# Kernel tuning notes

Measured on AMD Instinct MI355X. Metric: run time of the kernel, lower is better.

## Reference

```python
import jax, jax.numpy as jnp
import numpy as np

E = 200000
T = 1000000
D = 128          # embed_dim
NB = 20          # n_basis (use_sh=False -> SimpleMLPAngleExpansion)


def setup_inputs() -> dict:
    key = jax.random.key(0)
    ks = jax.random.split(key, 16)
    s = lambda fan_in: 1.0 / np.sqrt(fan_in)
    return {
        "edge_attr": jax.random.normal(ks[0], (E, D), dtype=jnp.float32),
        "three_body_indices": jax.random.randint(ks[1], (T, 3), 0, 50000),
        "three_body_edge_indices": jax.random.randint(ks[2], (T, 2), 0, E),
        "edge_vectors": jax.random.normal(ks[3], (E, 3), dtype=jnp.float32),
        # SimpleMLPAngleExpansion: (len_ij, len_ik, cos) -> n_basis via 2-layer MLP
        "A1": jax.random.uniform(ks[4], (3, NB), jnp.float32, -s(3), s(3)),
        "ab1": jnp.zeros((NB,), jnp.float32),
        "A2": jax.random.uniform(ks[5], (NB, NB), jnp.float32, -s(NB), s(NB)),
        "ab2": jnp.zeros((NB,), jnp.float32),
        # phi_3b: Linear(2D+NB, D) -> SiLU -> Linear(D, D)
        "W1": jax.random.uniform(ks[6], (2 * D + NB, D), jnp.float32, -s(2 * D + NB), s(2 * D + NB)),
        "b1": jnp.zeros((D,), jnp.float32),
        "W2": jax.random.uniform(ks[7], (D, D), jnp.float32, -s(D), s(D)),
        "b2": jnp.zeros((D,), jnp.float32),
        # update_edge: Linear(D, D)
        "Wu": jax.random.uniform(ks[8], (D, D), jnp.float32, -s(D), s(D)),
        "bu": jnp.zeros((D,), jnp.float32),
    }


def reference(edge_attr, three_body_indices, three_body_edge_indices, edge_vectors,
              A1, ab1, A2, ab2, W1, b1, W2, b2, Wu, bu):
    e_ij = three_body_edge_indices[:, 0]
    e_ik = three_body_edge_indices[:, 1]
    vec_ij = -edge_vectors[e_ij]          # (T, 3)
    vec_ik = -edge_vectors[e_ik]          # (T, 3)
    len_ij = jnp.clip(jnp.linalg.norm(vec_ij, axis=1, keepdims=True), 1e-6)
    len_ik = jnp.clip(jnp.linalg.norm(vec_ik, axis=1, keepdims=True), 1e-6)
    cos = jnp.clip(jnp.sum(vec_ij * vec_ik, axis=1, keepdims=True) / (len_ij * len_ik), -1.0, 1.0)
    # angle expansion (SimpleMLPAngleExpansion): small MLP on geometric scalars
    f = jnp.concatenate([len_ij, len_ik, cos], axis=-1)       # (T, 3)
    angle_feats = jax.nn.silu(f @ A1 + ab1) @ A2 + ab2         # (T, NB)
    h_3b = jnp.concatenate([edge_attr[e_ij], edge_attr[e_ik], angle_feats], axis=-1)  # (T, 2D+NB)
    m_ijk = jax.nn.silu(h_3b @ W1 + b1) @ W2 + b2              # (T, D)
    delta = jax.ops.segment_sum(m_ijk, e_ij, num_segments=edge_attr.shape[0])  # (E, D)
    return delta @ Wu + bu
```

## Files before the change

### kernel.cpp

```cpp
#include <hip/hip_runtime.h>
#include <stdint.h>

#define D_ 128
#define NB_ 20
#define SCAN_B 1024
#define SEG_BLOCKS 2048
#define NWAVES (SEG_BLOCKS * 256 / 64)

typedef __bf16 bf16x8 __attribute__((ext_vector_type(8)));
typedef float f32x4 __attribute__((ext_vector_type(4)));
typedef float f32x2 __attribute__((ext_vector_type(2)));

__device__ __forceinline__ float silu_f(float x) {
  return x * __builtin_amdgcn_rcpf(1.0f + __expf(-x));
}
__device__ __forceinline__ f32x2 silu2(f32x2 x) {
  return (f32x2){silu_f(x.x), silu_f(x.y)};
}
__device__ __forceinline__ f32x2 fsplat(float x) { return (f32x2){x, x}; }

__device__ __forceinline__ float bf2f(unsigned short u) {
  return __uint_as_float(((unsigned int)u) << 16);
}
__device__ __forceinline__ unsigned short f2bf(float f) {
  unsigned int x = __float_as_uint(f);
  return (unsigned short)((x + 0x7fffu + ((x >> 16) & 1u)) >> 16);
}

__global__ __launch_bounds__(256) void prep_kernel(
    const float* __restrict__ A2, const float* __restrict__ ab2,
    const float* __restrict__ W1, const float* __restrict__ b1,
    const float* __restrict__ W2, const float* __restrict__ Wu,
    const float* __restrict__ b2,
    float* __restrict__ Mfold, float* __restrict__ b1p,
    unsigned short* __restrict__ W2uT, float* __restrict__ c2,
    unsigned short* __restrict__ W1T) {
  int tid = blockIdx.x * blockDim.x + threadIdx.x;
  if (tid < 21 * D_) {
    int r = tid >> 7, c = tid & (D_ - 1);
    if (r < NB_) {
      float acc = 0.f;
      for (int j = 0; j < NB_; ++j) acc += A2[r * NB_ + j] * W1[(2 * D_ + j) * D_ + c];
      Mfold[r * D_ + c] = acc;
    } else {
      float acc = b1[c];
      for (int j = 0; j < NB_; ++j) acc += ab2[j] * W1[(2 * D_ + j) * D_ + c];
      b1p[c] = acc;
    }
  } else if (tid < 2688 + 16384) {
    int i = tid - 2688;
    int n = i >> 7, k = i & 127;
    float acc = 0.f;
    for (int m = 0; m < D_; ++m) acc += W2[k * D_ + m] * Wu[m * D_ + n];
    W2uT[i] = f2bf(acc);
  } else if (tid < 19072 + 128) {
    int n = tid - 19072;
    float acc = 0.f;
    for (int m = 0; m < D_; ++m) acc += b2[m] * Wu[m * D_ + n];
    c2[n] = acc;
  } else if (tid < 19200 + 32768) {
    int i = tid - 19200;
    int r = i >> 7, k = i & 127;
    int half = r >> 7, n = r & 127;
    W1T[i] = f2bf(W1[(size_t)(half * 128 + k) * D_ + n]);
  }
}

__global__ __launch_bounds__(256) void pq_mfma(const float* __restrict__ edge_attr,
                                               const unsigned short* __restrict__ W1T,
                                               unsigned short* __restrict__ P,
                                               unsigned short* __restrict__ Q, int E) {
  const int lane = threadIdx.x & 63;
  const int wave = threadIdx.x >> 6;
  const int e0 = (blockIdx.x * 4 + wave) * 16;
  if (e0 >= E) return;
  const int row = lane & 15;
  const int quad = lane >> 4;
  int e = e0 + row; if (e >= E) e = E - 1;

  union { bf16x8 v; unsigned short u[8]; } afr[4];
  const float* arow = edge_attr + (size_t)e * D_ + quad * 8;
#pragma unroll
  for (int kt = 0; kt < 4; ++kt) {
    float4 f0 = *(const float4*)(arow + kt * 32);
    float4 f1 = *(const float4*)(arow + kt * 32 + 4);
    afr[kt].u[0] = f2bf(f0.x); afr[kt].u[1] = f2bf(f0.y);
    afr[kt].u[2] = f2bf(f0.z); afr[kt].u[3] = f2bf(f0.w);
    afr[kt].u[4] = f2bf(f1.x); afr[kt].u[5] = f2bf(f1.y);
    afr[kt].u[6] = f2bf(f1.z); afr[kt].u[7] = f2bf(f1.w);
  }
#pragma unroll
  for (int half = 0; half < 2; ++half) {
    unsigned short* Obase = half ? Q : P;
#pragma unroll
    for (int nt = 0; nt < 8; ++nt) {
      const unsigned short* wrow =
          W1T + ((size_t)(half * 128 + nt * 16 + row)) * 128 + quad * 8;
      f32x4 acc = {0.f, 0.f, 0.f, 0.f};
#pragma unroll
      for (int kt = 0; kt < 4; ++kt) {
        bf16x8 bfr = *(const bf16x8*)(wrow + kt * 32);
        acc = __builtin_amdgcn_mfma_f32_16x16x32_bf16(afr[kt].v, bfr, acc, 0, 0, 0);
      }
      int n = nt * 16 + row;
#pragma unroll
      for (int i = 0; i < 4; ++i) {
        int er = e0 + quad * 4 + i;
        if (er < E) Obase[(size_t)er * D_ + n] = f2bf(acc[i]);
      }
    }
  }
}

__global__ void hist_kernel(const int* __restrict__ tbe, int* __restrict__ cnt, int T_) {
  int t = blockIdx.x * blockDim.x + threadIdx.x;
  if (t < T_) atomicAdd(&cnt[((const int2*)tbe)[t].x], 1);
}

__global__ __launch_bounds__(SCAN_B) void scan1_kernel(const int* __restrict__ cnt,
                                                       int* __restrict__ pre,
                                                       int* __restrict__ bsum, int E) {
  __shared__ int lds[SCAN_B];
  int tid = threadIdx.x, i = blockIdx.x * SCAN_B + tid;
  int v = (i < E) ? cnt[i] : 0;
  lds[tid] = v;
  __syncthreads();
  for (int d = 1; d < SCAN_B; d <<= 1) {
    int add = (tid >= d) ? lds[tid - d] : 0;
    __syncthreads();
    lds[tid] += add;
    __syncthreads();
  }
  if (i < E) pre[i] = lds[tid] - v;
  if (tid == SCAN_B - 1) bsum[blockIdx.x] = lds[tid];
}

__global__ void scan2_kernel(int* __restrict__ bsum, int nb) {
  __shared__ int lds[256];
  int tid = threadIdx.x;
  int v = (tid < nb) ? bsum[tid] : 0;
  lds[tid] = v;
  __syncthreads();
  for (int d = 1; d < 256; d <<= 1) {
    int add = (tid >= d) ? lds[tid - d] : 0;
    __syncthreads();
    lds[tid] += add;
    __syncthreads();
  }
  if (tid < nb) bsum[tid] = lds[tid] - v;
}

__global__ __launch_bounds__(SCAN_B) void scan3_kernel(const int* __restrict__ pre,
                                                       const int* __restrict__ bsum,
                                                       int* __restrict__ offs,
                                                       int* __restrict__ cursor, int E, int T_) {
  int i = blockIdx.x * SCAN_B + threadIdx.x;
  if (i < E) {
    int o = pre[i] + bsum[blockIdx.x];
    offs[i] = o;
    cursor[i] = o;
  }
  if (i == 0) offs[E] = T_;
}

__global__ __launch_bounds__(256) void wfill_kernel(const int* __restrict__ offs,
                                                    int* __restrict__ wstart,
                                                    int E, int T_, int NW) {
  int e = blockIdx.x * blockDim.x + threadIdx.x;
  if (e >= E) return;
  unsigned long long a = (unsigned long long)offs[e] * (unsigned long long)NW;
  unsigned long long b = (unsigned long long)offs[e + 1] * (unsigned long long)NW;
  int w_lo = (int)((a + T_ - 1) / (unsigned long long)T_);
  int w_hi = (int)((b + T_ - 1) / (unsigned long long)T_);
  for (int w = w_lo; w < w_hi; ++w) wstart[w] = e;
}

__global__ void scatter_kernel(const int* __restrict__ tbe, int* __restrict__ cursor,
                               const float* __restrict__ edge_vectors,
                               const float* __restrict__ A1, const float* __restrict__ ab1,
                               int* __restrict__ seik, float* __restrict__ gT, int T_) {
  int t = blockIdx.x * blockDim.x + threadIdx.x;
  if (t >= T_) return;
  int2 v = ((const int2*)tbe)[t];
  int pos = atomicAdd(&cursor[v.x], 1);
  seik[pos] = v.y;
  const float* vj = edge_vectors + 3 * (size_t)v.x;
  const float* vk = edge_vectors + 3 * (size_t)v.y;
  float jx = vj[0], jy = vj[1], jz = vj[2];
  float kx = vk[0], ky = vk[1], kz = vk[2];
  float lij = fmaxf(__builtin_amdgcn_sqrtf(jx * jx + jy * jy + jz * jz), 1e-6f);
  float lik = fmaxf(__builtin_amdgcn_sqrtf(kx * kx + ky * ky + kz * kz), 1e-6f);
  float cosv = (jx * kx + jy * ky + jz * kz) * __builtin_amdgcn_rcpf(lij * lik);
  cosv = fminf(fmaxf(cosv, -1.f), 1.f);
  union { float4 v4[5]; float f[NB_]; } gr;
#pragma unroll
  for (int k = 0; k < NB_; ++k)
    gr.f[k] = silu_f(lij * A1[k] + lik * A1[NB_ + k] + cosv * A1[2 * NB_ + k] + ab1[k]);
  float4* gp = (float4*)(gT + (size_t)pos * NB_);
#pragma unroll
  for (int i = 0; i < 5; ++i) gp[i] = gr.v4[i];
}

struct G5 { float4 a, b, c, d, e; };

__device__ __forceinline__ G5 loadG(const char* __restrict__ gc, int t) {
  const float4* p = (const float4*)(
      gc + 80u * (unsigned)__builtin_amdgcn_readfirstlane(t));
  G5 g;
  g.a = p[0]; g.b = p[1]; g.c = p[2]; g.d = p[3]; g.e = p[4];
  return g;
}

__device__ __forceinline__ void body_acc(f32x2& acc, const f32x2 base,
                                         const G5& G, ushort2 qq,
                                         const f32x2* __restrict__ m) {
  const float* Gf = (const float*)&G;
  f32x2 u = base + (f32x2){bf2f(qq.x), bf2f(qq.y)};
  f32x2 ub = fsplat(0.f);
#pragma unroll
  for (int k = 0; k < NB_; k += 2) {
    u  += fsplat(Gf[k])     * m[k];
    ub += fsplat(Gf[k + 1]) * m[k + 1];
  }
  u += ub;
  acc += silu2(u);
}

__global__ __launch_bounds__(256, 6) void seg_kernel(
    const int* __restrict__ offs, const int* __restrict__ seik,
    const float* __restrict__ gT,
    const float* __restrict__ Mfold, const float* __restrict__ b1p,
    const unsigned short* __restrict__ P, const unsigned short* __restrict__ Q,
    const int* __restrict__ wstart,
    float* __restrict__ s_out, int E, int NW) {
  const int lane = threadIdx.x & 63;
  const int w = __builtin_amdgcn_readfirstlane(
      (int)((blockIdx.x * blockDim.x + threadIdx.x) >> 6));
  if (w >= NW) return;

  f32x2 m[NB_];
#pragma unroll
  for (int k = 0; k < NB_; ++k) {
    float2 t2 = *(const float2*)(Mfold + k * D_ + 2 * lane);
    m[k] = (f32x2){t2.x, t2.y};
  }
  const float2 bbt = *(const float2*)(b1p + 2 * lane);
  const f32x2 bb = (f32x2){bbt.x, bbt.y};

  int es = (w == 0) ? 0 : wstart[w];
  int ee = (w == NW - 1) ? E : wstart[w + 1];
  if (es >= ee) return;

  const char* Qc = (const char*)Q;
  const char* Pc = (const char*)P;
  const char* gc = (const char*)gT;
  const unsigned loff = (unsigned)lane * 4u;

  int e = es;
  int t = offs[es];
  const int tend = offs[ee];
  int nxt = offs[es + 1];

  ushort2 pp = *(const ushort2*)(Pc + ((unsigned)e << 8) + loff);
  int epn = (e + 1 < E) ? e + 1 : E - 1;
  ushort2 ppn = *(const ushort2*)(Pc + ((unsigned)epn << 8) + loff);
  f32x2 base = (f32x2){bf2f(pp.x), bf2f(pp.y)} + bb;
  f32x2 acc = (f32x2){0.f, 0.f};

  if (t < tend) {
    int ek0 = seik[t], ek1 = seik[t + 1], ek2 = seik[t + 2], ek3 = seik[t + 3];
    ushort2 q0 = *(const ushort2*)(Qc + ((unsigned)ek0 << 8) + loff);
    ushort2 q1 = *(const ushort2*)(Qc + ((unsigned)ek1 << 8) + loff);
    ushort2 q2 = *(const ushort2*)(Qc + ((unsigned)ek2 << 8) + loff);
    ushort2 q3 = *(const ushort2*)(Qc + ((unsigned)ek3 << 8) + loff);
    int ekA = seik[t + 4], ekB = seik[t + 5], ekC = seik[t + 6], ekD = seik[t + 7];
    G5 Ga = loadG(gc, t);
    G5 Gb = loadG(gc, t + 1);

    while (t < tend) {
      while (t == nxt) {
        *(f32x2*)(s_out + (size_t)e * D_ + 2 * lane) = acc;
        acc = (f32x2){0.f, 0.f};
        ++e;
        nxt = offs[e + 1];
        base = (f32x2){bf2f(ppn.x), bf2f(ppn.y)} + bb;
        int ep = (e + 1 < E) ? e + 1 : E - 1;
        ppn = *(const ushort2*)(Pc + ((unsigned)ep << 8) + loff);
      }
      body_acc(acc, base, Ga, q0, m);
      q0 = q1; q1 = q2; q2 = q3;
      q3 = *(const ushort2*)(Qc + ((unsigned)ekA << 8) + loff);
      ekA = ekB; ekB = ekC; ekC = ekD; ekD = seik[t + 8];
      Ga = loadG(gc, t + 2);
      ++t;
      if (t >= tend) break;
      while (t == nxt) {
        *(f32x2*)(s_out + (size_t)e * D_ + 2 * lane) = acc;
        acc = (f32x2){0.f, 0.f};
        ++e;
        nxt = offs[e + 1];
        base = (f32x2){bf2f(ppn.x), bf2f(ppn.y)} + bb;
        int ep = (e + 1 < E) ? e + 1 : E - 1;
        ppn = *(const ushort2*)(Pc + ((unsigned)ep << 8) + loff);
      }
      body_acc(acc, base, Gb, q0, m);
      q0 = q1; q1 = q2; q2 = q3;
      q3 = *(const ushort2*)(Qc + ((unsigned)ekA << 8) + loff);
      ekA = ekB; ekB = ekC; ekC = ekD; ekD = seik[t + 8];
      Gb = loadG(gc, t + 2);
      ++t;
    }
  }
  while (e < ee) {
    *(f32x2*)(s_out + (size_t)e * D_ + 2 * lane) = acc;
    acc = (f32x2){0.f, 0.f};
    ++e;
  }
}

__global__ __launch_bounds__(256) void out_mfma(float* __restrict__ io,
                                                const unsigned short* __restrict__ W2uT,
                                                const float* __restrict__ c2,
                                                const float* __restrict__ bu,
                                                const int* __restrict__ cnt, int E) {
  const int lane = threadIdx.x & 63;
  const int wave = threadIdx.x >> 6;
  const int e0 = (blockIdx.x * 4 + wave) * 16;
  if (e0 >= E) return;
  const int row = lane & 15;
  const int quad = lane >> 4;
  int e = e0 + row; if (e >= E) e = E - 1;

  union { bf16x8 v; unsigned short u[8]; } afr[4];
  const float* arow = io + (size_t)e * D_ + quad * 8;
#pragma unroll
  for (int kt = 0; kt < 4; ++kt) {
    float4 f0 = *(const float4*)(arow + kt * 32);
    float4 f1 = *(const float4*)(arow + kt * 32 + 4);
    afr[kt].u[0] = f2bf(f0.x); afr[kt].u[1] = f2bf(f0.y);
    afr[kt].u[2] = f2bf(f0.z); afr[kt].u[3] = f2bf(f0.w);
    afr[kt].u[4] = f2bf(f1.x); afr[kt].u[5] = f2bf(f1.y);
    afr[kt].u[6] = f2bf(f1.z); afr[kt].u[7] = f2bf(f1.w);
  }
  float nf[4];
#pragma unroll
  for (int i = 0; i < 4; ++i) {
    int er = e0 + quad * 4 + i;
    nf[i] = (float)cnt[(er < E) ? er : (E - 1)];
  }
#pragma unroll
  for (int nt = 0; nt < 8; ++nt) {
    const unsigned short* wrow = W2uT + ((size_t)(nt * 16 + row)) * 128 + quad * 8;
    f32x4 acc = {0.f, 0.f, 0.f, 0.f};
#pragma unroll
    for (int kt = 0; kt < 4; ++kt) {
      bf16x8 bfr = *(const bf16x8*)(wrow + kt * 32);
      acc = __builtin_amdgcn_mfma_f32_16x16x32_bf16(afr[kt].v, bfr, acc, 0, 0, 0);
    }
    int n = nt * 16 + row;
    float c2n = c2[n], bun = bu[n];
#pragma unroll
    for (int i = 0; i < 4; ++i) {
      int er = e0 + quad * 4 + i;
      if (er < E) io[(size_t)er * D_ + n] = acc[i] + nf[i] * c2n + bun;
    }
  }
}

extern "C" void kernel_launch(void* const* d_in, const int* in_sizes, int n_in,
                              void* d_out, int out_size, void* d_ws, size_t ws_size,
                              hipStream_t stream) {
  const float* edge_attr    = (const float*)d_in[0];
  const int*   tbe          = (const int*)d_in[2];
  const float* edge_vectors = (const float*)d_in[3];
  const float* A1  = (const float*)d_in[4];
  const float* ab1 = (const float*)d_in[5];
  const float* A2  = (const float*)d_in[6];
  const float* ab2 = (const float*)d_in[7];
  const float* W1  = (const float*)d_in[8];
  const float* b1  = (const float*)d_in[9];
  const float* W2  = (const float*)d_in[10];
  const float* b2  = (const float*)d_in[11];
  const float* Wu  = (const float*)d_in[12];
  const float* bu  = (const float*)d_in[13];
  const int E = in_sizes[0] / D_;
  const int T = in_sizes[2] / 2;
  float* out = (float*)d_out;

  char* w = (char*)d_ws;
  auto carve = [&](size_t bytes) -> char* {
    char* p = w;
    w += (bytes + 255) & ~(size_t)255;
    return p;
  };
  unsigned short* P = (unsigned short*)carve((size_t)E * D_ * 2);
  unsigned short* Q = (unsigned short*)carve((size_t)E * D_ * 2);
  float* gT   = (float*)carve(((size_t)T + 8) * NB_ * 4);
  int* seik   = (int*)carve(((size_t)T + 8) * 4);
  int* cnt    = (int*)carve((size_t)E * 4);
  int* pre    = (int*)carve((size_t)E * 4);
  int* offs   = (int*)carve((size_t)(E + 1) * 4);
  int* cursor = (int*)carve((size_t)E * 4);
  int* bsum   = (int*)carve(1024 * 4);
  int* wstart = (int*)carve((size_t)NWAVES * 4);
  float* Mfold = (float*)carve(NB_ * D_ * 4);
  float* b1p   = (float*)carve(D_ * 4);
  unsigned short* W2uT = (unsigned short*)carve(D_ * D_ * 2);
  float* c2    = (float*)carve(D_ * 4);
  unsigned short* W1T = (unsigned short*)carve(256 * 128 * 2);

  const int nb_scan = (E + SCAN_B - 1) / SCAN_B;

  hipMemsetAsync(cnt, 0, (size_t)E * 4, stream);
  hipMemsetAsync(seik + T, 0, 8 * 4, stream);

  prep_kernel<<<(51968 + 255) / 256, 256, 0, stream>>>(A2, ab2, W1, b1, W2, Wu, b2,
                                                       Mfold, b1p, W2uT, c2, W1T);
  pq_mfma<<<(E + 63) / 64, 256, 0, stream>>>(edge_attr, W1T, P, Q, E);

  hist_kernel<<<(T + 255) / 256, 256, 0, stream>>>(tbe, cnt, T);
  scan1_kernel<<<nb_scan, SCAN_B, 0, stream>>>(cnt, pre, bsum, E);
  scan2_kernel<<<1, 256, 0, stream>>>(bsum, nb_scan);
  scan3_kernel<<<nb_scan, SCAN_B, 0, stream>>>(pre, bsum, offs, cursor, E, T);
  wfill_kernel<<<(E + 255) / 256, 256, 0, stream>>>(offs, wstart, E, T, NWAVES);
  scatter_kernel<<<(T + 255) / 256, 256, 0, stream>>>(tbe, cursor, edge_vectors,
                                                      A1, ab1, seik, gT, T);

  seg_kernel<<<SEG_BLOCKS, 256, 0, stream>>>(offs, seik, gT, Mfold, b1p, P, Q,
                                             wstart, out, E, NWAVES);
  out_mfma<<<(E + 63) / 64, 256, 0, stream>>>(out, W2uT, c2, bu, cnt, E);
}
```

Baseline: 695.0 us.

## Split geometry from scatter and store segment sums as bf16

The scatter kernel now writes only (e_ik, e_ij) pairs in sorted order. A new geom_kernel reads those sorted pairs and computes the angle features, so the gT writes become sequential instead of scattered. The segment-sum kernel stores per-edge accumulators as bf16 into the output buffer, and out_mfma loads them directly as MFMA operands, which halves that intermediate traffic and drops the float-to-bf16 conversion. The cost is an extra kernel launch, a wider seik array, and bf16 rounding of the segment sums, which the previous code already applied before the MFMA.

```diff
diff --git a/kernel.cpp b/kernel.cpp
--- a/kernel.cpp
+++ b/kernel.cpp
@@ -176,16 +176,24 @@
 }
 
 __global__ void scatter_kernel(const int* __restrict__ tbe, int* __restrict__ cursor,
-                               const float* __restrict__ edge_vectors,
-                               const float* __restrict__ A1, const float* __restrict__ ab1,
-                               int* __restrict__ seik, float* __restrict__ gT, int T_) {
+                               int2* __restrict__ seik2, int T_) {
   int t = blockIdx.x * blockDim.x + threadIdx.x;
   if (t >= T_) return;
   int2 v = ((const int2*)tbe)[t];
   int pos = atomicAdd(&cursor[v.x], 1);
-  seik[pos] = v.y;
-  const float* vj = edge_vectors + 3 * (size_t)v.x;
-  const float* vk = edge_vectors + 3 * (size_t)v.y;
+  seik2[pos] = make_int2(v.y, v.x);
+}
+
+__global__ __launch_bounds__(256) void geom_kernel(const int2* __restrict__ seik2,
+                                                   const float* __restrict__ edge_vectors,
+                                                   const float* __restrict__ A1,
+                                                   const float* __restrict__ ab1,
+                                                   float* __restrict__ gT, int T_) {
+  int t = blockIdx.x * blockDim.x + threadIdx.x;
+  if (t >= T_) return;
+  int2 s = seik2[t];
+  const float* vj = edge_vectors + 3 * (size_t)s.y;
+  const float* vk = edge_vectors + 3 * (size_t)s.x;
   float jx = vj[0], jy = vj[1], jz = vj[2];
   float kx = vk[0], ky = vk[1], kz = vk[2];
   float lij = fmaxf(__builtin_amdgcn_sqrtf(jx * jx + jy * jy + jz * jz), 1e-6f);
@@ -196,7 +204,7 @@
 #pragma unroll
   for (int k = 0; k < NB_; ++k)
     gr.f[k] = silu_f(lij * A1[k] + lik * A1[NB_ + k] + cosv * A1[2 * NB_ + k] + ab1[k]);
-  float4* gp = (float4*)(gT + (size_t)pos * NB_);
+  float4* gp = (float4*)(gT + (size_t)t * NB_);
 #pragma unroll
   for (int i = 0; i < 5; ++i) gp[i] = gr.v4[i];
 }
@@ -227,12 +235,12 @@
 }
 
 __global__ __launch_bounds__(256, 6) void seg_kernel(
-    const int* __restrict__ offs, const int* __restrict__ seik,
+    const int* __restrict__ offs, const int2* __restrict__ seik2,
     const float* __restrict__ gT,
     const float* __restrict__ Mfold, const float* __restrict__ b1p,
     const unsigned short* __restrict__ P, const unsigned short* __restrict__ Q,
     const int* __restrict__ wstart,
-    float* __restrict__ s_out, int E, int NW) {
+    char* __restrict__ s_out, int E, int NW) {
   const int lane = threadIdx.x & 63;
   const int w = __builtin_amdgcn_readfirstlane(
       (int)((blockIdx.x * blockDim.x + threadIdx.x) >> 6));
@@ -268,18 +276,19 @@
   f32x2 acc = (f32x2){0.f, 0.f};
 
   if (t < tend) {
-    int ek0 = seik[t], ek1 = seik[t + 1], ek2 = seik[t + 2], ek3 = seik[t + 3];
+    int ek0 = seik2[t].x, ek1 = seik2[t + 1].x, ek2 = seik2[t + 2].x, ek3 = seik2[t + 3].x;
     ushort2 q0 = *(const ushort2*)(Qc + ((unsigned)ek0 << 8) + loff);
     ushort2 q1 = *(const ushort2*)(Qc + ((unsigned)ek1 << 8) + loff);
     ushort2 q2 = *(const ushort2*)(Qc + ((unsigned)ek2 << 8) + loff);
     ushort2 q3 = *(const ushort2*)(Qc + ((unsigned)ek3 << 8) + loff);
-    int ekA = seik[t + 4], ekB = seik[t + 5], ekC = seik[t + 6], ekD = seik[t + 7];
+    int ekA = seik2[t + 4].x, ekB = seik2[t + 5].x, ekC = seik2[t + 6].x, ekD = seik2[t + 7].x;
     G5 Ga = loadG(gc, t);
     G5 Gb = loadG(gc, t + 1);
 
     while (t < tend) {
       while (t == nxt) {
-        *(f32x2*)(s_out + (size_t)e * D_ + 2 * lane) = acc;
+        *(ushort2*)(s_out + ((size_t)e << 9) + loff) =
+            make_ushort2(f2bf(acc.x), f2bf(acc.y));
         acc = (f32x2){0.f, 0.f};
         ++e;
         nxt = offs[e + 1];
@@ -290,12 +299,14 @@
       body_acc(acc, base, Ga, q0, m);
       q0 = q1; q1 = q2; q2 = q3;
       q3 = *(const ushort2*)(Qc + ((unsigned)ekA << 8) + loff);
-      ekA = ekB; ekB = ekC; ekC = ekD; ekD = seik[t + 8];
+      ekA = ekB; ekB = ekC; ekC = ekD;
+      ekD = seik2[__builtin_amdgcn_readfirstlane(t + 8)].x;
       Ga = loadG(gc, t + 2);
       ++t;
       if (t >= tend) break;
       while (t == nxt) {
-        *(f32x2*)(s_out + (size_t)e * D_ + 2 * lane) = acc;
+        *(ushort2*)(s_out + ((size_t)e << 9) + loff) =
+            make_ushort2(f2bf(acc.x), f2bf(acc.y));
         acc = (f32x2){0.f, 0.f};
         ++e;
         nxt = offs[e + 1];
@@ -306,13 +317,15 @@
       body_acc(acc, base, Gb, q0, m);
       q0 = q1; q1 = q2; q2 = q3;
       q3 = *(const ushort2*)(Qc + ((unsigned)ekA << 8) + loff);
-      ekA = ekB; ekB = ekC; ekC = ekD; ekD = seik[t + 8];
+      ekA = ekB; ekB = ekC; ekC = ekD;
+      ekD = seik2[__builtin_amdgcn_readfirstlane(t + 8)].x;
       Gb = loadG(gc, t + 2);
       ++t;
     }
   }
   while (e < ee) {
-    *(f32x2*)(s_out + (size_t)e * D_ + 2 * lane) = acc;
+    *(ushort2*)(s_out + ((size_t)e << 9) + loff) =
+        make_ushort2(f2bf(acc.x), f2bf(acc.y));
     acc = (f32x2){0.f, 0.f};
     ++e;
   }
@@ -331,17 +344,12 @@
   const int quad = lane >> 4;
   int e = e0 + row; if (e >= E) e = E - 1;
 
-  union { bf16x8 v; unsigned short u[8]; } afr[4];
-  const float* arow = io + (size_t)e * D_ + quad * 8;
-#pragma unroll
-  for (int kt = 0; kt < 4; ++kt) {
-    float4 f0 = *(const float4*)(arow + kt * 32);
-    float4 f1 = *(const float4*)(arow + kt * 32 + 4);
-    afr[kt].u[0] = f2bf(f0.x); afr[kt].u[1] = f2bf(f0.y);
-    afr[kt].u[2] = f2bf(f0.z); afr[kt].u[3] = f2bf(f0.w);
-    afr[kt].u[4] = f2bf(f1.x); afr[kt].u[5] = f2bf(f1.y);
-    afr[kt].u[6] = f2bf(f1.z); afr[kt].u[7] = f2bf(f1.w);
-  }
+  bf16x8 afr[4];
+  const char* arow = (const char*)io + ((size_t)e << 9) + quad * 16;
+#pragma unroll
+  for (int kt = 0; kt < 4; ++kt)
+    afr[kt] = *(const bf16x8*)(arow + kt * 64);
+
   float nf[4];
 #pragma unroll
   for (int i = 0; i < 4; ++i) {
@@ -355,7 +363,7 @@
 #pragma unroll
     for (int kt = 0; kt < 4; ++kt) {
       bf16x8 bfr = *(const bf16x8*)(wrow + kt * 32);
-      acc = __builtin_amdgcn_mfma_f32_16x16x32_bf16(afr[kt].v, bfr, acc, 0, 0, 0);
+      acc = __builtin_amdgcn_mfma_f32_16x16x32_bf16(afr[kt], bfr, acc, 0, 0, 0);
     }
     int n = nt * 16 + row;
     float c2n = c2[n], bun = bu[n];
@@ -396,7 +404,7 @@
   unsigned short* P = (unsigned short*)carve((size_t)E * D_ * 2);
   unsigned short* Q = (unsigned short*)carve((size_t)E * D_ * 2);
   float* gT   = (float*)carve(((size_t)T + 8) * NB_ * 4);
-  int* seik   = (int*)carve(((size_t)T + 8) * 4);
+  int2* seik2 = (int2*)carve(((size_t)T + 8) * 8);
   int* cnt    = (int*)carve((size_t)E * 4);
   int* pre    = (int*)carve((size_t)E * 4);
   int* offs   = (int*)carve((size_t)(E + 1) * 4);
@@ -412,7 +420,7 @@
   const int nb_scan = (E + SCAN_B - 1) / SCAN_B;
 
   hipMemsetAsync(cnt, 0, (size_t)E * 4, stream);
-  hipMemsetAsync(seik + T, 0, 8 * 4, stream);
+  hipMemsetAsync(seik2 + T, 0, 8 * 8, stream);
 
   prep_kernel<<<(51968 + 255) / 256, 256, 0, stream>>>(A2, ab2, W1, b1, W2, Wu, b2,
                                                        Mfold, b1p, W2uT, c2, W1T);
@@ -423,10 +431,10 @@
   scan2_kernel<<<1, 256, 0, stream>>>(bsum, nb_scan);
   scan3_kernel<<<nb_scan, SCAN_B, 0, stream>>>(pre, bsum, offs, cursor, E, T);
   wfill_kernel<<<(E + 255) / 256, 256, 0, stream>>>(offs, wstart, E, T, NWAVES);
-  scatter_kernel<<<(T + 255) / 256, 256, 0, stream>>>(tbe, cursor, edge_vectors,
-                                                      A1, ab1, seik, gT, T);
-
-  seg_kernel<<<SEG_BLOCKS, 256, 0, stream>>>(offs, seik, gT, Mfold, b1p, P, Q,
-                                             wstart, out, E, NWAVES);
+  scatter_kernel<<<(T + 255) / 256, 256, 0, stream>>>(tbe, cursor, seik2, T);
+  geom_kernel<<<(T + 255) / 256, 256, 0, stream>>>(seik2, edge_vectors, A1, ab1, gT, T);
+
+  seg_kernel<<<SEG_BLOCKS, 256, 0, stream>>>(offs, seik2, gT, Mfold, b1p, P, Q,
+                                             wstart, (char*)out, E, NWAVES);
   out_mfma<<<(E + 63) / 64, 256, 0, stream>>>(out, W2uT, c2, bu, cnt, E);
 }
```

Result: no change. 686.8 us (-1.2%).
